# Kernel tuning notes

Hardware: AMD Instinct MI355X
Metric: run time of the kernel (lower is better)

The kernel has to match this reference:

```python
import jax, jax.numpy as jnp
import numpy as np

B, N, D, H = 4, 1024, 768, 12
DH = D // H
HIDDEN = 4 * D
EPS = 1e-6


def _layernorm(x, g, b):
    mu = jnp.mean(x, axis=-1, keepdims=True)
    var = jnp.mean(jnp.square(x - mu), axis=-1, keepdims=True)
    return (x - mu) * jax.lax.rsqrt(var + EPS) * g + b


def setup_inputs() -> dict:
    key = jax.random.key(0)
    ks = jax.random.split(key, 8)
    s = 0.02  # init scale for weights
    return {
        "x": jax.random.normal(ks[0], (B, N, D), jnp.float32),
        "adj_bias": jax.random.normal(ks[1], (N, N), jnp.float32) * 0.1,
        "ln1_g": jnp.ones((D,), jnp.float32),
        "ln1_b": jnp.zeros((D,), jnp.float32),
        "qkv_w": jax.random.normal(ks[2], (D, 3 * D), jnp.float32) * s,
        "qkv_b": jnp.zeros((3 * D,), jnp.float32),
        "proj_w": jax.random.normal(ks[3], (D, D), jnp.float32) * s,
        "proj_b": jnp.zeros((D,), jnp.float32),
        "ln2_g": jnp.ones((D,), jnp.float32),
        "ln2_b": jnp.zeros((D,), jnp.float32),
        "fc1_w": jax.random.normal(ks[4], (D, HIDDEN), jnp.float32) * s,
        "fc1_b": jnp.zeros((HIDDEN,), jnp.float32),
        "fc2_w": jax.random.normal(ks[5], (HIDDEN, D), jnp.float32) * s,
        "fc2_b": jnp.zeros((D,), jnp.float32),
    }


def reference(x, adj_bias, ln1_g, ln1_b, qkv_w, qkv_b, proj_w, proj_b,
              ln2_g, ln2_b, fc1_w, fc1_b, fc2_w, fc2_b):
    scale = DH ** -0.5
    # --- attention with additive adjacency bias ---
    h = _layernorm(x, ln1_g, ln1_b)
    qkv = (h @ qkv_w + qkv_b).reshape(B, N, 3, H, DH)
    q, k, v = (jnp.moveaxis(qkv, 2, 0)[i].transpose(0, 2, 1, 3) for i in range(3))  # [B,H,N,DH]
    scores = jnp.einsum('bhqd,bhkd->bhqk', q, k) * scale + adj_bias[None, None]
    w = jax.nn.softmax(scores, axis=-1)
    attn = jnp.einsum('bhqk,bhkd->bhqd', w, v)          # [B,H,N,DH]
    attn = attn.transpose(0, 2, 1, 3).reshape(B, N, D)  # [B,N,D]
    x = x + (attn @ proj_w + proj_b)
    # --- MLP ---
    h2 = _layernorm(x, ln2_g, ln2_b)
    m = jax.nn.gelu(h2 @ fc1_w + fc1_b, approximate=False) @ fc2_w + fc2_b
    return x + m
```

## Files before the change

kernel.cpp:

```cpp
#include <hip/hip_runtime.h>
#include <cstdint>
#include <cstring>

typedef unsigned short u16;
typedef __attribute__((ext_vector_type(8))) short short8;
typedef __attribute__((ext_vector_type(4))) float float4v;

#define BB 4
#define NN 1024
#define DD 768
#define HH 12
#define DHH 64
#define HID 3072
#define MM (BB*NN)

__device__ __forceinline__ u16 f2b(float f) {
  unsigned int u = __float_as_uint(f);
  u += 0x7FFF + ((u >> 16) & 1);
  return (u16)(u >> 16);
}
__device__ __forceinline__ float b2f(u16 h) {
  return __uint_as_float(((unsigned int)h) << 16);
}

__device__ __forceinline__ void gll16(const void* g, void* l) {
  __builtin_amdgcn_global_load_lds(
      (const __attribute__((address_space(1))) unsigned int*)g,
      (__attribute__((address_space(3))) unsigned int*)l, 16, 0, 0);
}

__global__ __launch_bounds__(256)
void front_k(const float* __restrict__ qkvw, const float* __restrict__ projw,
             const float* __restrict__ fc1w, const float* __restrict__ fc2w,
             const float* __restrict__ adj, const float* __restrict__ x,
             const float* __restrict__ ln1g, const float* __restrict__ ln1b,
             u16* __restrict__ wtqkv, u16* __restrict__ wtproj,
             u16* __restrict__ wtfc1, u16* __restrict__ wtfc2,
             u16* __restrict__ adjP, u16* __restrict__ hbuf) {
  __shared__ float tile[32][33];
  __shared__ float rs[4], rs2[4], bc[2];
  const int id = blockIdx.x, t = threadIdx.x;
  if (id < 6912) {
    const float* w; u16* wt; int K, N, tid;
    if (id < 1728)      { w = qkvw;  wt = wtqkv;  K = DD;  N = 3 * DD; tid = id; }
    else if (id < 2304) { w = projw; wt = wtproj; K = DD;  N = DD;     tid = id - 1728; }
    else if (id < 4608) { w = fc1w;  wt = wtfc1;  K = DD;  N = HID;    tid = id - 2304; }
    else                { w = fc2w;  wt = wtfc2;  K = HID; N = DD;     tid = id - 4608; }
    const int ntiles = N / 32;
    const int n0 = (tid % ntiles) * 32, k0 = (tid / ntiles) * 32;
    const int tx = t & 31, ty = t >> 5;
#pragma unroll
    for (int i = 0; i < 4; i++)
      tile[ty + i * 8][tx] = w[(size_t)(k0 + ty + i * 8) * N + n0 + tx];
    __syncthreads();
#pragma unroll
    for (int i = 0; i < 4; i++)
      wt[(size_t)(n0 + ty + i * 8) * K + k0 + tx] = f2b(tile[tx][ty + i * 8]);
  } else if (id < 7168) {
    const int aid = id - 6912;
    const int qt = aid >> 4, kt = aid & 15;
    const int wv = t >> 6, q4 = (t >> 4) & 3, m15 = t & 15;
    u16 v[16];
#pragma unroll
    for (int ct = 0; ct < 4; ct++)
#pragma unroll
      for (int r = 0; r < 4; r++)
        v[ct * 4 + r] =
            f2b(adj[(size_t)(qt * 64 + wv * 16 + q4 * 4 + r) * NN + kt * 64 + ct * 16 + m15]);
    u16* dst = adjP + (size_t)aid * 4096 + t * 16;
    *(uint4*)dst = *(const uint4*)&v[0];
    *(uint4*)(dst + 8) = *(const uint4*)&v[8];
  } else {
    const int row = id - 7168;
    const float* xr = x + (size_t)row * DD;
    float v0 = xr[t], v1 = xr[t + 256], v2 = xr[t + 512];
    float s = v0 + v1 + v2;
    float s2 = v0 * v0 + v1 * v1 + v2 * v2;
#pragma unroll
    for (int off = 32; off > 0; off >>= 1) {
      s += __shfl_down(s, off);
      s2 += __shfl_down(s2, off);
    }
    const int lane = t & 63, wv = t >> 6;
    if (lane == 0) { rs[wv] = s; rs2[wv] = s2; }
    __syncthreads();
    if (t == 0) {
      float ts = rs[0] + rs[1] + rs[2] + rs[3];
      float ts2 = rs2[0] + rs2[1] + rs2[2] + rs2[3];
      float mean = ts * (1.f / DD);
      float var = ts2 * (1.f / DD) - mean * mean;
      bc[0] = mean;
      bc[1] = rsqrtf(var + 1e-6f);
    }
    __syncthreads();
    const float mean = bc[0], rstd = bc[1];
    u16* orow = hbuf + (size_t)row * DD;
    orow[t]       = f2b((v0 - mean) * rstd * ln1g[t]       + ln1b[t]);
    orow[t + 256] = f2b((v1 - mean) * rstd * ln1g[t + 256] + ln1b[t + 256]);
    orow[t + 512] = f2b((v2 - mean) * rstd * ln1g[t + 512] + ln1b[t + 512]);
  }
}

__global__ __launch_bounds__(256)
void ln_k(const float* __restrict__ x, const float* __restrict__ g,
          const float* __restrict__ b, u16* __restrict__ o) {
  const int row = blockIdx.x, t = threadIdx.x;
  const float* xr = x + (size_t)row * DD;
  float v0 = xr[t], v1 = xr[t + 256], v2 = xr[t + 512];
  float s = v0 + v1 + v2;
  float s2 = v0 * v0 + v1 * v1 + v2 * v2;
#pragma unroll
  for (int off = 32; off > 0; off >>= 1) {
    s += __shfl_down(s, off);
    s2 += __shfl_down(s2, off);
  }
  __shared__ float rs[4], rs2[4], bc[2];
  const int lane = t & 63, wv = t >> 6;
  if (lane == 0) { rs[wv] = s; rs2[wv] = s2; }
  __syncthreads();
  if (t == 0) {
    float ts = rs[0] + rs[1] + rs[2] + rs[3];
    float ts2 = rs2[0] + rs2[1] + rs2[2] + rs2[3];
    float mean = ts * (1.f / DD);
    float var = ts2 * (1.f / DD) - mean * mean;
    bc[0] = mean;
    bc[1] = rsqrtf(var + 1e-6f);
  }
  __syncthreads();
  const float mean = bc[0], rstd = bc[1];
  u16* orow = o + (size_t)row * DD;
  orow[t]       = f2b((v0 - mean) * rstd * g[t]       + b[t]);
  orow[t + 256] = f2b((v1 - mean) * rstd * g[t + 256] + b[t + 256]);
  orow[t + 512] = f2b((v2 - mean) * rstd * g[t + 512] + b[t + 512]);
}

template <int MODE, int TN, int BK, int NC>
__global__ __launch_bounds__(128, 2)
void gemm_k(const u16* __restrict__ A, const u16* __restrict__ Bt,
            const float* __restrict__ bias, const float* __restrict__ resid,
            float* __restrict__ outf, u16* __restrict__ outb,
            u16* __restrict__ outq, u16* __restrict__ outk, u16* __restrict__ outv,
            int K) {
  constexpr int BM = 64;
  __shared__ u16 smem[2 * BM * BK + 2 * TN * BK];
  constexpr int JM = TN / 32;
  constexpr int KK = BK / 32;
  constexpr int SLOTS = BK / 8;
  constexpr int AI = BM * SLOTS / 64;
  constexpr int BI = TN * SLOTS / 64;
  constexpr int VC = (AI + BI) / 2;
  constexpr int APT = AI / 2;
  constexpr int BPT = BI / 2;
  constexpr int NB = NC / TN;
  constexpr int RN = NB / 2;
  constexpr int MB = MM / BM;

  const int id = blockIdx.x;
  const int xcd = id & 7, idx = id >> 3;
  const int tileN = ((xcd & 1) * RN + idx % RN) * TN;
  const int tileM = ((xcd >> 1) * (MB / 4) + idx / RN) * BM;

  const int t = threadIdx.x;
  const int lane = t & 63, wave = t >> 6;
  const int wcol = wave * (TN / 2);
  const int m15 = lane & 15, q4 = lane >> 4;
  const int rkey = (BK == 32) ? ((m15 >> 1) & 3) : (m15 & 7);

  const u16* ag[APT]; int ao[APT];
  const u16* bg[BPT]; int bo[BPT];
#pragma unroll
  for (int qi = 0; qi < APT; qi++) {
    const int q = wave + 2 * qi;
    const int c = q * 64 + lane;
    const int row = c / SLOTS, slot = c % SLOTS;
    const int key = (BK == 32) ? ((row >> 1) & 3) : (row & 7);
    ag[qi] = A + (size_t)(tileM + row) * K + (slot ^ key) * 8;
    ao[qi] = q * 512;
  }
#pragma unroll
  for (int qi = 0; qi < BPT; qi++) {
    const int q = wave + 2 * qi;
    const int c = q * 64 + lane;
    const int row = c / SLOTS, slot = c % SLOTS;
    const int key = (BK == 32) ? ((row >> 1) & 3) : (row & 7);
    bg[qi] = Bt + (size_t)(tileN + row) * K + (slot ^ key) * 8;
    bo[qi] = q * 512;
  }

  float4v acc[4][JM];
#pragma unroll
  for (int i = 0; i < 4; i++)
#pragma unroll
    for (int j = 0; j < JM; j++) acc[i][j] = (float4v)0.f;

  auto stage = [&](int buf) {
#pragma unroll
    for (int qi = 0; qi < APT; qi++)
      gll16(ag[qi], smem + buf * (BM * BK) + ao[qi]);
#pragma unroll
    for (int qi = 0; qi < BPT; qi++)
      gll16(bg[qi], smem + 2 * (BM * BK) + buf * (TN * BK) + bo[qi]);
#pragma unroll
    for (int qi = 0; qi < APT; qi++) ag[qi] += BK;
#pragma unroll
    for (int qi = 0; qi < BPT; qi++) bg[qi] += BK;
  };

  const int T = K / BK;
  stage(0);
  for (int kt = 0; kt < T; ++kt) {
    const int cur = kt & 1;
    if (kt + 1 < T) {
      stage(cur ^ 1);
      asm volatile("s_waitcnt vmcnt(%0)\n\ts_barrier" :: "n"(VC) : "memory");
    } else {
      asm volatile("s_waitcnt vmcnt(0)\n\ts_barrier" ::: "memory");
    }
    const u16* As = smem + cur * (BM * BK);
    const u16* Bs = smem + 2 * (BM * BK) + cur * (TN * BK);
    short8 af[4][KK], bfr[JM][KK];
#pragma unroll
    for (int i = 0; i < 4; i++)
#pragma unroll
      for (int kk = 0; kk < KK; kk++)
        af[i][kk] = *(const short8*)(
            As + (i * 16 + m15) * BK + (((kk * 4 + q4) ^ rkey)) * 8);
#pragma unroll
    for (int j = 0; j < JM; j++)
#pragma unroll
      for (int kk = 0; kk < KK; kk++)
        bfr[j][kk] = *(const short8*)(
            Bs + (wcol + j * 16 + m15) * BK + (((kk * 4 + q4) ^ rkey)) * 8);
#pragma unroll
    for (int i = 0; i < 4; i++)
#pragma unroll
      for (int j = 0; j < JM; j++)
#pragma unroll
        for (int kk = 0; kk < KK; kk++)
          acc[i][j] =
              __builtin_amdgcn_mfma_f32_16x16x32_bf16(af[i][kk], bfr[j][kk], acc[i][j], 0, 0, 0);
    asm volatile("s_waitcnt lgkmcnt(0)\n\ts_barrier" ::: "memory");
  }

  if constexpr (MODE == 1) {
#pragma unroll
    for (int i = 0; i < 4; i++) {
#pragma unroll
      for (int j = 0; j < JM; j++) {
        const int col = tileN + wcol + j * 16 + m15;
#pragma unroll
        for (int r = 0; r < 4; r++) {
          const int row = tileM + i * 16 + q4 * 4 + r;
          float v = acc[i][j][r] + bias[col];
          outf[(size_t)row * NC + col] = resid[(size_t)row * NC + col] + v;
        }
      }
    }
  } else {
    const bool isv = (MODE == 0) && (tileN >= 2 * DD);
    u16* cs = smem;
    if (!isv) {
      constexpr int CP = TN + 8;
#pragma unroll
      for (int i = 0; i < 4; i++)
#pragma unroll
        for (int j = 0; j < JM; j++) {
          const int col = wcol + j * 16 + m15;
          const float bi = bias[tileN + col];
#pragma unroll
          for (int r = 0; r < 4; r++) {
            float v = acc[i][j][r] + bi;
            if (MODE == 2) v = 0.5f * v * (1.f + erff(v * 0.70710678f));
            cs[(i * 16 + q4 * 4 + r) * CP + col] = f2b(v);
          }
        }
      __syncthreads();
#pragma unroll
      for (int p = 0; p < BM * (TN / 8) / 128; p++) {
        const int e = p * 128 + t;
        const int row = e >> 4, ch = e & 15;
        uint4 w = *(const uint4*)&cs[row * CP + ch * 8];
        if (MODE == 2) {
          *(uint4*)&outb[(size_t)(tileM + row) * NC + tileN + ch * 8] = w;
        } else {
          const int col0 = tileN + ch * 8;
          const int three = col0 / DD, hh = (col0 % DD) >> 6, dh0 = col0 & 63;
          const int grow = tileM + row, bb = grow >> 10, nn = grow & 1023;
          u16* dst = (three == 0 ? outq : outk) +
                     (((size_t)(bb * HH + hh)) * NN + nn) * DHH + dh0;
          *(uint4*)dst = w;
        }
      }
    } else {
      constexpr int CPV = BM + 8;
#pragma unroll
      for (int i = 0; i < 4; i++)
#pragma unroll
        for (int j = 0; j < JM; j++) {
          const int col = wcol + j * 16 + m15;
          const float bi = bias[tileN + col];
          u16 pk[4];
#pragma unroll
          for (int r = 0; r < 4; r++) pk[r] = f2b(acc[i][j][r] + bi);
          *(uint2*)&cs[col * CPV + i * 16 + q4 * 4] = *(const uint2*)pk;
        }
      __syncthreads();
#pragma unroll
      for (int p = 0; p < TN * (BM / 8) / 128; p++) {
        const int e = p * 128 + t;
        const int c = e >> 3, r0 = (e & 7) * 8;
        uint4 w = *(const uint4*)&cs[c * CPV + r0];
        const int col0 = tileN + c;
        const int hh = (col0 % DD) >> 6, dh = col0 & 63;
        const int grow = tileM + r0, bb = grow >> 10, nn0 = grow & 1023;
        *(uint4*)&outv[(((size_t)(bb * HH + hh)) * DHH + dh) * NN + nn0] = w;
      }
    }
  }
}

__global__ __launch_bounds__(256, 4)
void attn_k(const u16* __restrict__ qw, const u16* __restrict__ kw,
            const u16* __restrict__ vtw, const u16* __restrict__ adjP,
            u16* __restrict__ out) {
  __shared__ u16 Ks[64][72];
  __shared__ u16 Vt[64][72];
  __shared__ u16 Pb[4][16][72];

  const int id = blockIdx.x;
  const int bh = (id & 7) * 6 + ((id >> 3) >> 4);
  const int qt = (id >> 3) & 15;
  const int t = threadIdx.x, lane = t & 63, wave = t >> 6;
  const int m15 = lane & 15, q4 = lane >> 4;

  const u16* qrow = qw + ((size_t)bh * NN + qt * 64 + wave * 16 + m15) * DHH;
  const short8 qf0 = *(const short8*)(qrow + q4 * 8);
  const short8 qf1 = *(const short8*)(qrow + 32 + q4 * 8);

  float lreg[4] = {0.f, 0.f, 0.f, 0.f};
  float4v o[4];
#pragma unroll
  for (int ct = 0; ct < 4; ct++) o[ct] = (float4v)0.f;

  const u16* kbase0 = kw + (size_t)bh * NN * DHH;
  const u16* vtbase0 = vtw + (size_t)bh * DHH * NN;
  const u16* abase = adjP + (size_t)qt * 16 * 4096 + t * 16;

  const int r0 = t >> 3;
  const int c80 = (t & 7) * 8;

  uint4 kr0 = *(const uint4*)(kbase0 + r0 * 64 + c80);
  uint4 kr1 = *(const uint4*)(kbase0 + (r0 + 32) * 64 + c80);
  uint4 vr0 = *(const uint4*)(vtbase0 + (size_t)r0 * NN + c80);
  uint4 vr1 = *(const uint4*)(vtbase0 + (size_t)(r0 + 32) * NN + c80);

  for (int kt = 0; kt < 16; kt++) {
    __syncthreads();
    *(uint4*)&Ks[r0][c80] = kr0;
    *(uint4*)&Ks[r0 + 32][c80] = kr1;
    *(uint4*)&Vt[r0][c80] = vr0;
    *(uint4*)&Vt[r0 + 32][c80] = vr1;
    __syncthreads();
    if (kt < 15) {
      const u16* kb = kbase0 + (size_t)(kt + 1) * 64 * DHH;
      const u16* vb = vtbase0 + (kt + 1) * 64;
      kr0 = *(const uint4*)(kb + r0 * 64 + c80);
      kr1 = *(const uint4*)(kb + (r0 + 32) * 64 + c80);
      vr0 = *(const uint4*)(vb + (size_t)r0 * NN + c80);
      vr1 = *(const uint4*)(vb + (size_t)(r0 + 32) * NN + c80);
    }
    u16 av[16];
    const u16* ap = abase + (size_t)kt * 4096;
    *(uint4*)&av[0] = *(const uint4*)ap;
    *(uint4*)&av[8] = *(const uint4*)(ap + 8);

    float4v s[4];
#pragma unroll
    for (int ct = 0; ct < 4; ct++) s[ct] = (float4v)0.f;
#pragma unroll
    for (int ct = 0; ct < 4; ct++) {
      short8 b = *(const short8*)&Ks[ct * 16 + m15][q4 * 8];
      s[ct] = __builtin_amdgcn_mfma_f32_16x16x32_bf16(qf0, b, s[ct], 0, 0, 0);
    }
#pragma unroll
    for (int ct = 0; ct < 4; ct++) {
      short8 b = *(const short8*)&Ks[ct * 16 + m15][32 + q4 * 8];
      s[ct] = __builtin_amdgcn_mfma_f32_16x16x32_bf16(qf1, b, s[ct], 0, 0, 0);
    }

#pragma unroll
    for (int ct = 0; ct < 4; ct++)
#pragma unroll
      for (int r = 0; r < 4; r++) {
        float v = s[ct][r] * 0.125f + b2f(av[ct * 4 + r]);
        u16 pb = f2b(__expf(v));
        Pb[wave][q4 * 4 + r][ct * 16 + m15] = pb;
        lreg[r] += b2f(pb);
      }

    asm volatile("s_waitcnt lgkmcnt(0)" ::: "memory");

    short8 a0 = *(const short8*)&Pb[wave][m15][q4 * 8];
    short8 a1 = *(const short8*)&Pb[wave][m15][32 + q4 * 8];
#pragma unroll
    for (int ct = 0; ct < 4; ct++) {
      short8 b = *(const short8*)&Vt[ct * 16 + m15][q4 * 8];
      o[ct] = __builtin_amdgcn_mfma_f32_16x16x32_bf16(a0, b, o[ct], 0, 0, 0);
    }
#pragma unroll
    for (int ct = 0; ct < 4; ct++) {
      short8 b = *(const short8*)&Vt[ct * 16 + m15][32 + q4 * 8];
      o[ct] = __builtin_amdgcn_mfma_f32_16x16x32_bf16(a1, b, o[ct], 0, 0, 0);
    }
  }

#pragma unroll
  for (int off = 1; off < 16; off <<= 1)
#pragma unroll
    for (int r = 0; r < 4; r++) lreg[r] += __shfl_xor(lreg[r], off);

  const int bb2 = bh / HH, hh = bh % HH;
  const int row0 = qt * 64 + wave * 16 + q4 * 4;
#pragma unroll
  for (int ct = 0; ct < 4; ct++)
#pragma unroll
    for (int r = 0; r < 4; r++)
      out[((size_t)(bb2 * NN + row0 + r)) * DD + hh * 64 + ct * 16 + m15] =
          f2b(o[ct][r] / lreg[r]);
}

extern "C" void kernel_launch(void* const* d_in, const int* in_sizes, int n_in,
                              void* d_out, int out_size, void* d_ws, size_t ws_size,
                              hipStream_t stream) {
  const float* x     = (const float*)d_in[0];
  const float* adj   = (const float*)d_in[1];
  const float* ln1g  = (const float*)d_in[2];
  const float* ln1b  = (const float*)d_in[3];
  const float* qkvw  = (const float*)d_in[4];
  const float* qkvb  = (const float*)d_in[5];
  const float* projw = (const float*)d_in[6];
  const float* projb = (const float*)d_in[7];
  const float* ln2g  = (const float*)d_in[8];
  const float* ln2b  = (const float*)d_in[9];
  const float* fc1w  = (const float*)d_in[10];
  const float* fc1b  = (const float*)d_in[11];
  const float* fc2w  = (const float*)d_in[12];
  const float* fc2b  = (const float*)d_in[13];
  float* out = (float*)d_out;

  char* ws = (char*)d_ws;
  u16* wtqkv = (u16*)ws;  ws += (size_t)DD * (3 * DD) * 2;
  u16* wtproj = (u16*)ws; ws += (size_t)DD * DD * 2;
  u16* wtfc1 = (u16*)ws;  ws += (size_t)DD * HID * 2;
  u16* wtfc2 = (u16*)ws;  ws += (size_t)HID * DD * 2;
  u16* adjP = (u16*)ws;   ws += (size_t)NN * NN * 2;
  u16* hbuf = (u16*)ws;   ws += (size_t)MM * DD * 2;
  u16* qws = (u16*)ws;    ws += (size_t)MM * DD * 2;
  u16* kws = (u16*)ws;    ws += (size_t)MM * DD * 2;
  u16* vtws = (u16*)ws;   ws += (size_t)MM * DD * 2;
  u16* attnb = (u16*)ws;  ws += (size_t)MM * DD * 2;
  u16* h2buf = (u16*)ws;  ws += (size_t)MM * DD * 2;
  u16* a1buf = (u16*)ws;  ws += (size_t)MM * HID * 2;

  front_k<<<7168 + MM, 256, 0, stream>>>(qkvw, projw, fc1w, fc2w, adj, x, ln1g, ln1b,
                                         wtqkv, wtproj, wtfc1, wtfc2, adjP, hbuf);

  gemm_k<0, 128, 32, 3 * DD><<<((3 * DD) / 128) * (MM / 64), 128, 0, stream>>>(
      hbuf, wtqkv, qkvb, nullptr, nullptr, nullptr, qws, kws, vtws, DD);

  attn_k<<<(NN / 64) * (BB * HH), 256, 0, stream>>>(qws, kws, vtws, adjP, attnb);

  gemm_k<1, 64, 64, DD><<<(DD / 64) * (MM / 64), 128, 0, stream>>>(
      attnb, wtproj, projb, x, out, nullptr, nullptr, nullptr, nullptr, DD);

  ln_k<<<MM, 256, 0, stream>>>(out, ln2g, ln2b, h2buf);

  gemm_k<2, 128, 32, HID><<<(HID / 128) * (MM / 64), 128, 0, stream>>>(
      h2buf, wtfc1, fc1b, nullptr, nullptr, a1buf, nullptr, nullptr, nullptr, DD);

  gemm_k<1, 64, 64, DD><<<(DD / 64) * (MM / 64), 128, 0, stream>>>(
      a1buf, wtfc2, fc2b, out, out, nullptr, nullptr, nullptr, nullptr, HID);
}
```

Before: 260.8 us.

## Add 8-wave triple-buffered 128x256 GEMM for QKV and FC1 projections

```diff
diff --git a/kernel.cpp b/kernel.cpp
--- a/kernel.cpp
+++ b/kernel.cpp
@@ -138,9 +138,7 @@
 __global__ __launch_bounds__(128, 2)
 void gemm_k(const u16* __restrict__ A, const u16* __restrict__ Bt,
             const float* __restrict__ bias, const float* __restrict__ resid,
-            float* __restrict__ outf, u16* __restrict__ outb,
-            u16* __restrict__ outq, u16* __restrict__ outk, u16* __restrict__ outv,
-            int K) {
+            float* __restrict__ outf, int K) {
   constexpr int BM = 64;
   __shared__ u16 smem[2 * BM * BK + 2 * TN * BK];
   constexpr int JM = TN / 32;
@@ -242,79 +240,248 @@
     asm volatile("s_waitcnt lgkmcnt(0)\n\ts_barrier" ::: "memory");
   }
 
-  if constexpr (MODE == 1) {
-#pragma unroll
-    for (int i = 0; i < 4; i++) {
-#pragma unroll
-      for (int j = 0; j < JM; j++) {
-        const int col = tileN + wcol + j * 16 + m15;
+#pragma unroll
+  for (int i = 0; i < 4; i++) {
+#pragma unroll
+    for (int j = 0; j < JM; j++) {
+      const int col = tileN + wcol + j * 16 + m15;
+#pragma unroll
+      for (int r = 0; r < 4; r++) {
+        const int row = tileM + i * 16 + q4 * 4 + r;
+        float v = acc[i][j][r] + bias[col];
+        outf[(size_t)row * NC + col] = resid[(size_t)row * NC + col] + v;
+      }
+    }
+  }
+}
+
+template <int MODE, int NC>
+__global__ __launch_bounds__(512, 2)
+void gemm8p_k(const u16* __restrict__ A, const u16* __restrict__ Bt,
+              const float* __restrict__ bias, u16* __restrict__ outb,
+              u16* __restrict__ outq, u16* __restrict__ outk, u16* __restrict__ outv,
+              int K) {
+  constexpr int BM = 128, BN = 256, BK = 64;
+  constexpr int ASZ = BM * BK;
+  constexpr int BSZ = BN * BK;
+  constexpr int BUFSZ = ASZ + BSZ;
+  __shared__ u16 smem[3 * BUFSZ];
+  constexpr int MT = MM / BM;
+  constexpr int NT = NC / BN;
+  constexpr int NWG = MT * NT;
+
+  const int id = blockIdx.x;
+  const int wg = (id & 7) * (NWG / 8) + (id >> 3);
+  const int tileM = (wg % MT) * BM;
+  const int tileN = (wg / MT) * BN;
+
+  const int t = threadIdx.x;
+  const int lane = t & 63, w = t >> 6;
+  const int wm = w >> 2, wn = w & 3;
+  const int m15 = lane & 15, q4 = lane >> 4;
+  const int rkey = m15 & 7;
+
+  const u16* asrc[2]; int aoff[2];
+  const u16* bsrc[4]; int boff[4];
+#pragma unroll
+  for (int qi = 0; qi < 2; qi++) {
+    const int q = qi * 8 + w;
+    const int c = q * 64 + lane;
+    const int row = c >> 3, slot = c & 7;
+    asrc[qi] = A + (size_t)(tileM + row) * K + (slot ^ (row & 7)) * 8;
+    aoff[qi] = q * 512;
+  }
+#pragma unroll
+  for (int qi = 0; qi < 4; qi++) {
+    const int q = qi * 8 + w;
+    const int c = q * 64 + lane;
+    const int row = c >> 3, slot = c & 7;
+    bsrc[qi] = Bt + (size_t)(tileN + row) * K + (slot ^ (row & 7)) * 8;
+    boff[qi] = q * 512;
+  }
+
+  float4v acc[4][4];
+#pragma unroll
+  for (int i = 0; i < 4; i++)
+#pragma unroll
+    for (int j = 0; j < 4; j++) acc[i][j] = (float4v)0.f;
+
+  auto stageA = [&](int kt, int buf) {
+#pragma unroll
+    for (int qi = 0; qi < 2; qi++)
+      gll16(asrc[qi] + (size_t)kt * BK, smem + buf * BUFSZ + aoff[qi]);
+  };
+  auto stageB = [&](int kt, int buf, int first) {
+#pragma unroll
+    for (int qi = 0; qi < 2; qi++)
+      gll16(bsrc[first + qi] + (size_t)kt * BK,
+            smem + buf * BUFSZ + ASZ + boff[first + qi]);
+  };
+
+  const int T = K / BK;
+  stageA(0, 0); stageB(0, 0, 0); stageB(0, 0, 2);
+  stageA(1, 1); stageB(1, 1, 0); stageB(1, 1, 2);
+
+  int c = 0;
+  for (int kt = 0; kt < T; ++kt) {
+    if (kt + 1 < T)
+      asm volatile("s_waitcnt vmcnt(6)" ::: "memory");
+    else
+      asm volatile("s_waitcnt vmcnt(0)" ::: "memory");
+    __builtin_amdgcn_s_barrier();
+
+    const u16* Ab = smem + c * BUFSZ;
+    const u16* Bb = Ab + ASZ;
+    const int c2 = (c == 0) ? 2 : c - 1;
+    const bool pre = (kt + 2 < T);
+
+    const int ar0 = (wm * 64 + m15) * BK;
+    const int br0 = (wn * 64 + m15) * BK;
+    short8 a0, a1, a2, a3, b0, b1, b2, b3;
+
+    {
+      const int so = (q4 ^ rkey) * 8;
+      a0 = *(const short8*)(Ab + ar0 + 0 * 16 * BK + so);
+      a1 = *(const short8*)(Ab + ar0 + 1 * 16 * BK + so);
+      b0 = *(const short8*)(Bb + br0 + 0 * 16 * BK + so);
+      b1 = *(const short8*)(Bb + br0 + 1 * 16 * BK + so);
+      b2 = *(const short8*)(Bb + br0 + 2 * 16 * BK + so);
+      b3 = *(const short8*)(Bb + br0 + 3 * 16 * BK + so);
+    }
+    if (pre) stageA(kt + 2, c2);
+    __builtin_amdgcn_s_barrier();
+    __builtin_amdgcn_s_setprio(1);
+    acc[0][0] = __builtin_amdgcn_mfma_f32_16x16x32_bf16(a0, b0, acc[0][0], 0, 0, 0);
+    acc[0][1] = __builtin_amdgcn_mfma_f32_16x16x32_bf16(a0, b1, acc[0][1], 0, 0, 0);
+    acc[0][2] = __builtin_amdgcn_mfma_f32_16x16x32_bf16(a0, b2, acc[0][2], 0, 0, 0);
+    acc[0][3] = __builtin_amdgcn_mfma_f32_16x16x32_bf16(a0, b3, acc[0][3], 0, 0, 0);
+    acc[1][0] = __builtin_amdgcn_mfma_f32_16x16x32_bf16(a1, b0, acc[1][0], 0, 0, 0);
+    acc[1][1] = __builtin_amdgcn_mfma_f32_16x16x32_bf16(a1, b1, acc[1][1], 0, 0, 0);
+    acc[1][2] = __builtin_amdgcn_mfma_f32_16x16x32_bf16(a1, b2, acc[1][2], 0, 0, 0);
+    acc[1][3] = __builtin_amdgcn_mfma_f32_16x16x32_bf16(a1, b3, acc[1][3], 0, 0, 0);
+    __builtin_amdgcn_s_setprio(0);
+    __builtin_amdgcn_s_barrier();
+
+    {
+      const int so = (q4 ^ rkey) * 8;
+      a2 = *(const short8*)(Ab + ar0 + 2 * 16 * BK + so);
+      a3 = *(const short8*)(Ab + ar0 + 3 * 16 * BK + so);
+    }
+    if (pre) stageB(kt + 2, c2, 0);
+    __builtin_amdgcn_s_barrier();
+    __builtin_amdgcn_s_setprio(1);
+    acc[2][0] = __builtin_amdgcn_mfma_f32_16x16x32_bf16(a2, b0, acc[2][0], 0, 0, 0);
+    acc[2][1] = __builtin_amdgcn_mfma_f32_16x16x32_bf16(a2, b1, acc[2][1], 0, 0, 0);
+    acc[2][2] = __builtin_amdgcn_mfma_f32_16x16x32_bf16(a2, b2, acc[2][2], 0, 0, 0);
+    acc[2][3] = __builtin_amdgcn_mfma_f32_16x16x32_bf16(a2, b3, acc[2][3], 0, 0, 0);
+    acc[3][0] = __builtin_amdgcn_mfma_f32_16x16x32_bf16(a3, b0, acc[3][0], 0, 0, 0);
+    acc[3][1] = __builtin_amdgcn_mfma_f32_16x16x32_bf16(a3, b1, acc[3][1], 0, 0, 0);
+    acc[3][2] = __builtin_amdgcn_mfma_f32_16x16x32_bf16(a3, b2, acc[3][2], 0, 0, 0);
+    acc[3][3] = __builtin_amdgcn_mfma_f32_16x16x32_bf16(a3, b3, acc[3][3], 0, 0, 0);
+    __builtin_amdgcn_s_setprio(0);
+    __builtin_amdgcn_s_barrier();
+
+    {
+      const int so = ((4 + q4) ^ rkey) * 8;
+      a0 = *(const short8*)(Ab + ar0 + 0 * 16 * BK + so);
+      a1 = *(const short8*)(Ab + ar0 + 1 * 16 * BK + so);
+      b0 = *(const short8*)(Bb + br0 + 0 * 16 * BK + so);
+      b1 = *(const short8*)(Bb + br0 + 1 * 16 * BK + so);
+      b2 = *(const short8*)(Bb + br0 + 2 * 16 * BK + so);
+      b3 = *(const short8*)(Bb + br0 + 3 * 16 * BK + so);
+    }
+    if (pre) stageB(kt + 2, c2, 2);
+    __builtin_amdgcn_s_barrier();
+    __builtin_amdgcn_s_setprio(1);
+    acc[0][0] = __builtin_amdgcn_mfma_f32_16x16x32_bf16(a0, b0, acc[0][0], 0, 0, 0);
+    acc[0][1] = __builtin_amdgcn_mfma_f32_16x16x32_bf16(a0, b1, acc[0][1], 0, 0, 0);
+    acc[0][2] = __builtin_amdgcn_mfma_f32_16x16x32_bf16(a0, b2, acc[0][2], 0, 0, 0);
+    acc[0][3] = __builtin_amdgcn_mfma_f32_16x16x32_bf16(a0, b3, acc[0][3], 0, 0, 0);
+    acc[1][0] = __builtin_amdgcn_mfma_f32_16x16x32_bf16(a1, b0, acc[1][0], 0, 0, 0);
+    acc[1][1] = __builtin_amdgcn_mfma_f32_16x16x32_bf16(a1, b1, acc[1][1], 0, 0, 0);
+    acc[1][2] = __builtin_amdgcn_mfma_f32_16x16x32_bf16(a1, b2, acc[1][2], 0, 0, 0);
+    acc[1][3] = __builtin_amdgcn_mfma_f32_16x16x32_bf16(a1, b3, acc[1][3], 0, 0, 0);
+    __builtin_amdgcn_s_setprio(0);
+    __builtin_amdgcn_s_barrier();
+
+    {
+      const int so = ((4 + q4) ^ rkey) * 8;
+      a2 = *(const short8*)(Ab + ar0 + 2 * 16 * BK + so);
+      a3 = *(const short8*)(Ab + ar0 + 3 * 16 * BK + so);
+    }
+    __builtin_amdgcn_s_barrier();
+    __builtin_amdgcn_s_setprio(1);
+    acc[2][0] = __builtin_amdgcn_mfma_f32_16x16x32_bf16(a2, b0, acc[2][0], 0, 0, 0);
+    acc[2][1] = __builtin_amdgcn_mfma_f32_16x16x32_bf16(a2, b1, acc[2][1], 0, 0, 0);
+    acc[2][2] = __builtin_amdgcn_mfma_f32_16x16x32_bf16(a2, b2, acc[2][2], 0, 0, 0);
+    acc[2][3] = __builtin_amdgcn_mfma_f32_16x16x32_bf16(a2, b3, acc[2][3], 0, 0, 0);
+    acc[3][0] = __builtin_amdgcn_mfma_f32_16x16x32_bf16(a3, b0, acc[3][0], 0, 0, 0);
+    acc[3][1] = __builtin_amdgcn_mfma_f32_16x16x32_bf16(a3, b1, acc[3][1], 0, 0, 0);
+    acc[3][2] = __builtin_amdgcn_mfma_f32_16x16x32_bf16(a3, b2, acc[3][2], 0, 0, 0);
+    acc[3][3] = __builtin_amdgcn_mfma_f32_16x16x32_bf16(a3, b3, acc[3][3], 0, 0, 0);
+    __builtin_amdgcn_s_setprio(0);
+
+    c = (c == 2) ? 0 : c + 1;
+  }
+  __syncthreads();
+
+  const bool isv = (MODE == 0) && (tileN >= 2 * DD);
+  u16* cs = smem;
+  if (!isv) {
+    constexpr int CP = BN + 8;
+#pragma unroll
+    for (int i = 0; i < 4; i++)
+#pragma unroll
+      for (int j = 0; j < 4; j++) {
+        const int col = wn * 64 + j * 16 + m15;
+        const float bi = bias[tileN + col];
 #pragma unroll
         for (int r = 0; r < 4; r++) {
-          const int row = tileM + i * 16 + q4 * 4 + r;
-          float v = acc[i][j][r] + bias[col];
-          outf[(size_t)row * NC + col] = resid[(size_t)row * NC + col] + v;
+          float v = acc[i][j][r] + bi;
+          if (MODE == 2) v = 0.5f * v * (1.f + erff(v * 0.70710678f));
+          cs[(wm * 64 + i * 16 + q4 * 4 + r) * CP + col] = f2b(v);
         }
       }
+    __syncthreads();
+#pragma unroll
+    for (int p = 0; p < 8; p++) {
+      const int e = p * 512 + t;
+      const int row = e >> 5, ch = e & 31;
+      uint4 wv4 = *(const uint4*)&cs[row * CP + ch * 8];
+      if (MODE == 2) {
+        *(uint4*)&outb[(size_t)(tileM + row) * NC + tileN + ch * 8] = wv4;
+      } else {
+        const int col0 = tileN + ch * 8;
+        const int three = col0 / DD, hh = (col0 - three * DD) >> 6, dh0 = col0 & 63;
+        const int grow = tileM + row, bb = grow >> 10, nn = grow & 1023;
+        u16* dst = (three == 0 ? outq : outk) +
+                   (((size_t)(bb * HH + hh)) * NN + nn) * DHH + dh0;
+        *(uint4*)dst = wv4;
+      }
     }
   } else {
-    const bool isv = (MODE == 0) && (tileN >= 2 * DD);
-    u16* cs = smem;
-    if (!isv) {
-      constexpr int CP = TN + 8;
-#pragma unroll
-      for (int i = 0; i < 4; i++)
-#pragma unroll
-        for (int j = 0; j < JM; j++) {
-          const int col = wcol + j * 16 + m15;
-          const float bi = bias[tileN + col];
-#pragma unroll
-          for (int r = 0; r < 4; r++) {
-            float v = acc[i][j][r] + bi;
-            if (MODE == 2) v = 0.5f * v * (1.f + erff(v * 0.70710678f));
-            cs[(i * 16 + q4 * 4 + r) * CP + col] = f2b(v);
-          }
-        }
-      __syncthreads();
-#pragma unroll
-      for (int p = 0; p < BM * (TN / 8) / 128; p++) {
-        const int e = p * 128 + t;
-        const int row = e >> 4, ch = e & 15;
-        uint4 w = *(const uint4*)&cs[row * CP + ch * 8];
-        if (MODE == 2) {
-          *(uint4*)&outb[(size_t)(tileM + row) * NC + tileN + ch * 8] = w;
-        } else {
-          const int col0 = tileN + ch * 8;
-          const int three = col0 / DD, hh = (col0 % DD) >> 6, dh0 = col0 & 63;
-          const int grow = tileM + row, bb = grow >> 10, nn = grow & 1023;
-          u16* dst = (three == 0 ? outq : outk) +
-                     (((size_t)(bb * HH + hh)) * NN + nn) * DHH + dh0;
-          *(uint4*)dst = w;
-        }
+    constexpr int CPV = BM + 8;
+#pragma unroll
+    for (int i = 0; i < 4; i++)
+#pragma unroll
+      for (int j = 0; j < 4; j++) {
+        const int col = wn * 64 + j * 16 + m15;
+        const float bi = bias[tileN + col];
+        u16 pk[4];
+#pragma unroll
+        for (int r = 0; r < 4; r++) pk[r] = f2b(acc[i][j][r] + bi);
+        *(uint2*)&cs[col * CPV + wm * 64 + i * 16 + q4 * 4] = *(const uint2*)pk;
       }
-    } else {
-      constexpr int CPV = BM + 8;
-#pragma unroll
-      for (int i = 0; i < 4; i++)
-#pragma unroll
-        for (int j = 0; j < JM; j++) {
-          const int col = wcol + j * 16 + m15;
-          const float bi = bias[tileN + col];
-          u16 pk[4];
-#pragma unroll
-          for (int r = 0; r < 4; r++) pk[r] = f2b(acc[i][j][r] + bi);
-          *(uint2*)&cs[col * CPV + i * 16 + q4 * 4] = *(const uint2*)pk;
-        }
-      __syncthreads();
-#pragma unroll
-      for (int p = 0; p < TN * (BM / 8) / 128; p++) {
-        const int e = p * 128 + t;
-        const int c = e >> 3, r0 = (e & 7) * 8;
-        uint4 w = *(const uint4*)&cs[c * CPV + r0];
-        const int col0 = tileN + c;
-        const int hh = (col0 % DD) >> 6, dh = col0 & 63;
-        const int grow = tileM + r0, bb = grow >> 10, nn0 = grow & 1023;
-        *(uint4*)&outv[(((size_t)(bb * HH + hh)) * DHH + dh) * NN + nn0] = w;
-      }
+    __syncthreads();
+#pragma unroll
+    for (int p = 0; p < 8; p++) {
+      const int e = p * 512 + t;
+      const int cc = e >> 4, r0 = (e & 15) * 8;
+      uint4 wv4 = *(const uint4*)&cs[cc * CPV + r0];
+      const int col0 = tileN + cc;
+      const int hh = (col0 - 2 * DD) >> 6, dh = col0 & 63;
+      const int grow = tileM + r0, bb = grow >> 10, nn0 = grow & 1023;
+      *(uint4*)&outv[(((size_t)(bb * HH + hh)) * DHH + dh) * NN + nn0] = wv4;
     }
   }
 }
@@ -465,19 +632,19 @@
   front_k<<<7168 + MM, 256, 0, stream>>>(qkvw, projw, fc1w, fc2w, adj, x, ln1g, ln1b,
                                          wtqkv, wtproj, wtfc1, wtfc2, adjP, hbuf);
 
-  gemm_k<0, 128, 32, 3 * DD><<<((3 * DD) / 128) * (MM / 64), 128, 0, stream>>>(
-      hbuf, wtqkv, qkvb, nullptr, nullptr, nullptr, qws, kws, vtws, DD);
+  gemm8p_k<0, 3 * DD><<<(MM / 128) * ((3 * DD) / 256), 512, 0, stream>>>(
+      hbuf, wtqkv, qkvb, nullptr, qws, kws, vtws, DD);
 
   attn_k<<<(NN / 64) * (BB * HH), 256, 0, stream>>>(qws, kws, vtws, adjP, attnb);
 
   gemm_k<1, 64, 64, DD><<<(DD / 64) * (MM / 64), 128, 0, stream>>>(
-      attnb, wtproj, projb, x, out, nullptr, nullptr, nullptr, nullptr, DD);
+      attnb, wtproj, projb, x, out, DD);
 
   ln_k<<<MM, 256, 0, stream>>>(out, ln2g, ln2b, h2buf);
 
-  gemm_k<2, 128, 32, HID><<<(HID / 128) * (MM / 64), 128, 0, stream>>>(
-      h2buf, wtfc1, fc1b, nullptr, nullptr, a1buf, nullptr, nullptr, nullptr, DD);
+  gemm8p_k<2, HID><<<(MM / 128) * (HID / 256), 512, 0, stream>>>(
+      h2buf, wtfc1, fc1b, a1buf, nullptr, nullptr, nullptr, DD);
 
   gemm_k<1, 64, 64, DD><<<(DD / 64) * (MM / 64), 128, 0, stream>>>(
-      a1buf, wtfc2, fc2b, out, out, nullptr, nullptr, nullptr, nullptr, HID);
-}
+      a1buf, wtfc2, fc2b, out, out, HID);
+}
```

Result: no change. 265.2 us (+1.7%).
